# Optimization experiments

Hardware: AMD Instinct MI355X
Metric: run time of the kernel (lower is better)

The kernel has to match this reference:

```python
import jax, jax.numpy as jnp
import numpy as np

P_FACTOR = 3.0   # config['p_factor']
EPS = 1e-12      # torch F.normalize eps

def _l2_normalize(x):
    return x / jnp.maximum(jnp.linalg.norm(x, axis=-1, keepdims=True), EPS)

def _l1_normalize(x):
    return x / jnp.maximum(jnp.sum(jnp.abs(x), axis=-1, keepdims=True), EPS)

def setup_inputs() -> dict:
    key = jax.random.key(0)
    k = jax.random.split(key, 6)
    B, N_EX, D_IN, D_FEAT, N_LAB, D_CLS = 4096, 16384, 1024, 256, 28, 64
    features = jax.random.normal(k[0], (B, D_IN), jnp.float32)
    labels = jax.random.uniform(k[1], (B, N_LAB), jnp.float32)            # BCE targets in [0,1]
    ex_features = jax.random.normal(k[2], (N_EX, D_IN), jnp.float32)
    ex_classes = jax.random.uniform(k[3], (N_EX, N_LAB), jnp.float32)     # class memberships
    g_w = jax.random.normal(k[4], (D_FEAT, D_IN), jnp.float32) * 0.02     # Linear(in=1024,out=256,bias=False)
    class_reps = jax.random.uniform(k[5], (N_LAB, D_CLS), jnp.float32) * 2.0 - 1.0  # rand*2-1
    return {"features": features, "labels": labels, "ex_features": ex_features,
            "ex_classes": ex_classes, "g_w": g_w, "class_reps": class_reps}

def reference(features, labels, ex_features, ex_classes, g_w, class_reps):
    # g projection (use_g=True, no bias)
    f = features @ g_w.T          # [B, D_FEAT]
    ef = ex_features @ g_w.T      # [N_EX, D_FEAT]
    # exemplar class representations: L1-normalized memberships @ class_reps
    ex_class_reps = _l1_normalize(ex_classes) @ class_reps   # [N_EX, D_CLS]
    # cosine similarity between queries and exemplars
    s = _l2_normalize(f) @ _l2_normalize(ef).T               # [B, N_EX]
    # power-sign activation then L1 normalize over exemplars
    a = _l1_normalize(jnp.sign(s) * jnp.abs(s) ** P_FACTOR)  # [B, N_EX]
    # weighted exemplar aggregation
    echo = a @ ex_class_reps                                  # [B, D_CLS]
    # negative euclidean distances to class representations (cdist)
    diff = echo[:, None, :] - class_reps[None, :, :]          # [B, N_LAB, D_CLS]
    neg_dists = -jnp.sqrt(jnp.sum(diff * diff, axis=-1))      # [B, N_LAB]
    # BCEWithLogitsLoss (mean reduction)
    loss = jnp.mean(-(labels * jax.nn.log_sigmoid(neg_dists)
                      + (1.0 - labels) * jax.nn.log_sigmoid(-neg_dists)))
    return (loss, neg_dists)
```

## Files before the change

### kernel.cpp

```cpp
#include <hip/hip_runtime.h>


typedef __bf16 bf16x8 __attribute__((ext_vector_type(8)));
typedef __bf16 bf16x4 __attribute__((ext_vector_type(4)));
typedef float  f32x4  __attribute__((ext_vector_type(4)));

__device__ __forceinline__ f32x4 f4zero() { f32x4 z = {0.f, 0.f, 0.f, 0.f}; return z; }

__device__ __forceinline__ f32x4 mfma16(bf16x8 a, bf16x8 b, f32x4 c) {
  return __builtin_amdgcn_mfma_f32_16x16x32_bf16(a, b, c, 0, 0, 0);
}

__device__ __forceinline__ bf16x8 load8f(const float* p) {
  f32x4 a = *(const f32x4*)p;
  f32x4 b = *(const f32x4*)(p + 4);
  bf16x8 r;
  r[0] = (__bf16)a[0]; r[1] = (__bf16)a[1]; r[2] = (__bf16)a[2]; r[3] = (__bf16)a[3];
  r[4] = (__bf16)b[0]; r[5] = (__bf16)b[1]; r[6] = (__bf16)b[2]; r[7] = (__bf16)b[3];
  return r;
}

__device__ __forceinline__ void async16(const void* g, void* l) {
  __builtin_amdgcn_global_load_lds(
      (const __attribute__((address_space(1))) unsigned int*)g,
      (__attribute__((address_space(3))) unsigned int*)l, 16, 0, 0);
}

__device__ __forceinline__ void bar_lgkm() {
  asm volatile("s_waitcnt lgkmcnt(0)" ::: "memory");
  __builtin_amdgcn_s_barrier();
}
__device__ __forceinline__ void bar_all() {
  asm volatile("s_waitcnt vmcnt(0) lgkmcnt(0)" ::: "memory");
  __builtin_amdgcn_s_barrier();
}

__global__ void fill_sentinel(float* __restrict__ out, int n) {
  for (int i = blockIdx.x * 256 + threadIdx.x; i < n; i += gridDim.x * 256) out[i] = -1.0f;
}

__global__ void prep(const float* __restrict__ exc, __bf16* __restrict__ vT,
                     const float* __restrict__ W, __bf16* __restrict__ W2,
                     float* __restrict__ zp, int zn) {
  const int b = blockIdx.x, tid = threadIdx.x;
  if (b < 64) {
    int e = b * 256 + tid;
    float m[28];
    float s = 0.f;
#pragma unroll
    for (int j = 0; j < 28; j++) {
      m[j] = exc[(size_t)e * 28 + j];
      s += fabsf(m[j]);
    }
    float inv = 1.0f / fmaxf(s, 1e-12f);
#pragma unroll
    for (int j = 0; j < 28; j++) vT[(size_t)j * 16384 + e] = (__bf16)(m[j] * inv);
#pragma unroll
    for (int j = 28; j < 32; j++) vT[(size_t)j * 16384 + e] = (__bf16)0.0f;
  } else if (b < 192) {
    int i = (b - 64) * 256 + tid;
    int ks  = i >> 11;
    int idx = i & 2047;
    int row = idx >> 3;
    int c4  = (idx & 7) ^ (row & 7);
    *(bf16x8*)(W2 + (size_t)i * 8) = load8f(W + (size_t)row * 1024 + ks * 64 + c4 * 8);
  } else {
    for (int i = (b - 192) * 256 + tid; i < zn; i += (gridDim.x - 192) * 256) zp[i] = 0.f;
  }
}

__global__ __launch_bounds__(256, 2)
void proj_l2norm(const float* __restrict__ Xa, const float* __restrict__ Xb,
                 const __bf16* __restrict__ W2,
                 __bf16* __restrict__ Pa, __bf16* __restrict__ Pb) {
  __shared__ __align__(16) __bf16 Xs[2][32 * 72];
  __shared__ __align__(16) __bf16 Ws[2][256 * 64];
  __shared__ float nrmW[4 * 32];
  __shared__ float invn[32];

  const int tid = threadIdx.x;
  const int w = tid >> 6, lane = tid & 63;
  const int quad = lane >> 4, l15 = lane & 15;
  const int sw = l15 & 7;
  const int xrow = tid >> 3, xc8 = tid & 7;

  const float* X;
  __bf16* P;
  int row0;
  if (blockIdx.x < 512) { X = Xa; P = Pa; row0 = blockIdx.x * 32; }
  else                  { X = Xb; P = Pb; row0 = (blockIdx.x - 512) * 32; }

  const float* xsrc = X + (size_t)(row0 + xrow) * 1024 + xc8 * 8;

  *(bf16x8*)(&Xs[0][xrow * 72 + xc8 * 8]) = load8f(xsrc);
#pragma unroll
  for (int rep = 0; rep < 8; rep++) {
    int idx = rep * 256 + tid;
    async16(W2 + idx * 8, &Ws[0][idx * 8]);
  }

  f32x4 acc[2][4];
#pragma unroll
  for (int i = 0; i < 2; i++)
#pragma unroll
    for (int j = 0; j < 4; j++) acc[i][j] = f4zero();

  bar_all();

  int cur = 0;
  for (int ks = 0; ks < 16; ks++) {
    const int nxt = cur ^ 1;
    f32x4 xa, xb;
    if (ks < 15) {
      const float* xp = xsrc + (ks + 1) * 64;
      xa = *(const f32x4*)xp;
      xb = *(const f32x4*)(xp + 4);
      const __bf16* w2k = W2 + (size_t)(ks + 1) * 16384;
#pragma unroll
      for (int rep = 0; rep < 8; rep++) {
        int idx = rep * 256 + tid;
        async16(w2k + idx * 8, &Ws[nxt][idx * 8]);
      }
    }
#pragma unroll
    for (int ksub = 0; ksub < 2; ksub++) {
      bf16x8 af[2], bfr[4];
#pragma unroll
      for (int mb = 0; mb < 2; mb++)
        af[mb] = *(bf16x8*)(&Xs[cur][(mb * 16 + l15) * 72 + ksub * 32 + quad * 8]);
#pragma unroll
      for (int nb = 0; nb < 4; nb++) {
        int c4 = ksub * 4 + quad;
        bfr[nb] = *(bf16x8*)(&Ws[cur][(w * 64 + nb * 16 + l15) * 64 + (c4 ^ sw) * 8]);
      }
#pragma unroll
      for (int mb = 0; mb < 2; mb++)
#pragma unroll
        for (int nb = 0; nb < 4; nb++)
          acc[mb][nb] = mfma16(af[mb], bfr[nb], acc[mb][nb]);
    }
    if (ks < 15) {
      bf16x8 r;
      r[0] = (__bf16)xa[0]; r[1] = (__bf16)xa[1]; r[2] = (__bf16)xa[2]; r[3] = (__bf16)xa[3];
      r[4] = (__bf16)xb[0]; r[5] = (__bf16)xb[1]; r[6] = (__bf16)xb[2]; r[7] = (__bf16)xb[3];
      *(bf16x8*)(&Xs[nxt][xrow * 72 + xc8 * 8]) = r;
    }
    bar_all();
    cur = nxt;
  }

  float part[2][4];
#pragma unroll
  for (int mb = 0; mb < 2; mb++)
#pragma unroll
    for (int r = 0; r < 4; r++) {
      float s = 0.f;
#pragma unroll
      for (int nb = 0; nb < 4; nb++) { float v = acc[mb][nb][r]; s += v * v; }
      part[mb][r] = s;
    }
#pragma unroll
  for (int m = 1; m < 16; m <<= 1)
#pragma unroll
    for (int mb = 0; mb < 2; mb++)
#pragma unroll
      for (int r = 0; r < 4; r++) part[mb][r] += __shfl_xor(part[mb][r], m, 64);

  if (l15 == 0) {
#pragma unroll
    for (int mb = 0; mb < 2; mb++)
#pragma unroll
      for (int r = 0; r < 4; r++)
        nrmW[w * 32 + mb * 16 + quad * 4 + r] = part[mb][r];
  }
  __syncthreads();
  if (tid < 32) {
    float s = nrmW[tid] + nrmW[32 + tid] + nrmW[64 + tid] + nrmW[96 + tid];
    invn[tid] = 1.0f / fmaxf(sqrtf(s), 1e-12f);
  }
  __syncthreads();
#pragma unroll
  for (int mb = 0; mb < 2; mb++)
#pragma unroll
    for (int nb = 0; nb < 4; nb++)
#pragma unroll
      for (int r = 0; r < 4; r++) {
        int row = mb * 16 + quad * 4 + r;
        int col = w * 64 + nb * 16 + l15;
        P[(size_t)(row0 + row) * 256 + col] = (__bf16)(acc[mb][nb][r] * invn[row]);
      }
}

__global__ __launch_bounds__(256, 2)
void fused_sim(const __bf16* __restrict__ fn, const __bf16* __restrict__ efn,
               const __bf16* __restrict__ vTg,
               float* __restrict__ tT, float* __restrict__ r_acc) {
  __shared__ __align__(16) __bf16 Ks[64 * 256];
  __shared__ __align__(16) __bf16 Vs[2][32 * 64];
  __shared__ __align__(16) __bf16 Us[128 * 72];

  const int tid = threadIdx.x, w = tid >> 6, lane = tid & 63;
  const int quad = lane >> 4, l15 = lane & 15;
  const int wy = w >> 1, wx = w & 1;
  const int swk = l15 & 7;
  const int chunk = blockIdx.x & 15, mtile = blockIdx.x >> 4;
  const int q0 = mtile * 128;
  const int e_base = chunk * 1024;

  int koff[8];
#pragma unroll
  for (int rep = 0; rep < 8; rep++) {
    int idx = rep * 256 + tid;
    int row = idx >> 5;
    int c5  = (idx & 31) ^ (row & 7);
    koff[rep] = row * 256 + c5 * 8;
  }
  const int vrow = tid >> 3;
  const int vcs  = (tid & 7) ^ (vrow & 7);
  const size_t vsrc0 = (size_t)vrow * 16384 + e_base + vcs * 8;

  {
    const __bf16* src = efn + (size_t)e_base * 256;
#pragma unroll
    for (int rep = 0; rep < 8; rep++) async16(src + koff[rep], Ks + (rep * 256 + tid) * 8);
    async16(vTg + vsrc0, &Vs[0][tid * 8]);
  }

  bf16x8 qf[8][4];
#pragma unroll
  for (int ks = 0; ks < 8; ks++)
#pragma unroll
    for (int nb = 0; nb < 4; nb++)
      qf[ks][nb] = *(const bf16x8*)(fn + (size_t)(q0 + wx * 64 + nb * 16 + l15) * 256 +
                                    ks * 32 + quad * 8);

  float r_part[4] = {0.f, 0.f, 0.f, 0.f};
  f32x4 accp[2][2];
#pragma unroll
  for (int a = 0; a < 2; a++)
#pragma unroll
    for (int b = 0; b < 2; b++) accp[a][b] = f4zero();

  bar_all();

  int cur = 0;
  for (int t = 0; t < 16; t++) {
    f32x4 accs[2][4];
#pragma unroll
    for (int a = 0; a < 2; a++)
#pragma unroll
      for (int b = 0; b < 4; b++) accs[a][b] = f4zero();
#pragma unroll
    for (int ks = 0; ks < 8; ks++) {
      bf16x8 af[2];
#pragma unroll
      for (int mb = 0; mb < 2; mb++)
        af[mb] = *(bf16x8*)(Ks + (wy * 32 + mb * 16 + l15) * 256 +
                            ((ks * 4 + quad) ^ swk) * 8);
#pragma unroll
      for (int mb = 0; mb < 2; mb++)
#pragma unroll
        for (int nb = 0; nb < 4; nb++)
          accs[mb][nb] = mfma16(af[mb], qf[ks][nb], accs[mb][nb]);
    }

    bar_lgkm();

    if (t < 15) {
      const __bf16* src = efn + (size_t)(e_base + (t + 1) * 64) * 256;
#pragma unroll
      for (int rep = 0; rep < 8; rep++)
        async16(src + koff[rep], Ks + (rep * 256 + tid) * 8);
      async16(vTg + vsrc0 + (t + 1) * 64, &Vs[cur ^ 1][tid * 8]);
    }

#pragma unroll
    for (int mb = 0; mb < 2; mb++) {
      const int eo = wy * 32 + mb * 16 + quad * 4;
#pragma unroll
      for (int nb = 0; nb < 4; nb++) {
        const int q = wx * 64 + nb * 16 + l15;
        bf16x4 pk;
#pragma unroll
        for (int r = 0; r < 4; r++) {
          float s = accs[mb][nb][r];
          __bf16 ub = (__bf16)(s * s * s);
          pk[r] = ub;
          r_part[nb] += fabsf((float)ub);
        }
        *(bf16x4*)(Us + q * 72 + eo) = pk;
      }
    }

    bar_lgkm();

#pragma unroll
    for (int ks = 0; ks < 2; ks++) {
      bf16x8 vf[2], uf[2];
#pragma unroll
      for (int cb = 0; cb < 2; cb++)
        vf[cb] = *(bf16x8*)(&Vs[cur][(cb * 16 + l15) * 64 + ((ks * 4 + quad) ^ swk) * 8]);
#pragma unroll
      for (int qb = 0; qb < 2; qb++)
        uf[qb] = *(bf16x8*)(Us + (w * 32 + qb * 16 + l15) * 72 + ks * 32 + quad * 8);
#pragma unroll
      for (int cb = 0; cb < 2; cb++)
#pragma unroll
        for (int qb = 0; qb < 2; qb++)
          accp[cb][qb] = mfma16(vf[cb], uf[qb], accp[cb][qb]);
    }

    bar_all();
    cur ^= 1;
  }

#pragma unroll
  for (int nb = 0; nb < 4; nb++) {
    float v = r_part[nb];
    v += __shfl_xor(v, 16, 64);
    v += __shfl_xor(v, 32, 64);
    if (quad == 0) atomicAdd(&r_acc[q0 + wx * 64 + nb * 16 + l15], v);
  }
#pragma unroll
  for (int cb = 0; cb < 2; cb++)
#pragma unroll
    for (int qb = 0; qb < 2; qb++)
#pragma unroll
      for (int r = 0; r < 4; r++)
        atomicAdd(&tT[(size_t)(cb * 16 + quad * 4 + r) * 4096 + q0 + w * 32 + qb * 16 + l15],
                  accp[cb][qb][r]);
}

__global__ __launch_bounds__(256, 4)
void finalize(const float* __restrict__ tT, const float* __restrict__ r_acc,
              const float* __restrict__ creps, const float* __restrict__ labels,
              float* __restrict__ loss_acc, float* __restrict__ out) {
  __shared__ __align__(16) float cr[28 * 64];
  __shared__ float wsum[4];
  const int tid = threadIdx.x, w = tid >> 6, lane = tid & 63;
  for (int i = tid; i < 28 * 64; i += 256) cr[i] = creps[i];
  __syncthreads();

  const int q = blockIdx.x * 4 + w;
  float tval = 0.f;
  if (lane < 28) tval = tT[(size_t)lane * 4096 + q];
  tval *= 1.0f / fmaxf(r_acc[q], 1e-12f);

  float echo = 0.f;
#pragma unroll
  for (int j = 0; j < 28; j++)
    echo = fmaf(__shfl(tval, j, 64), cr[j * 64 + lane], echo);

  float dj = 0.f;
#pragma unroll
  for (int j = 0; j < 28; j++) {
    float df = echo - cr[j * 64 + lane];
    float d2 = df * df;
#pragma unroll
    for (int m = 1; m < 64; m <<= 1) d2 += __shfl_xor(d2, m, 64);
    if (lane == j) dj = sqrtf(d2);
  }

  float lsum = 0.f;
  if (lane < 28) {
    out[1 + (size_t)q * 28 + lane] = -dj;
    float y = labels[(size_t)q * 28 + lane];
    lsum = fmaf(y, dj, log1pf(expf(-dj)));
  }
#pragma unroll
  for (int m = 1; m < 64; m <<= 1) lsum += __shfl_xor(lsum, m, 64);
  if (lane == 0) wsum[w] = lsum;
  __syncthreads();
  if (tid == 0) atomicAdd(loss_acc, wsum[0] + wsum[1] + wsum[2] + wsum[3]);
}

__global__ void write_loss(const float* __restrict__ loss_acc, float* __restrict__ out) {
  out[0] = loss_acc[0] * (1.0f / 114688.0f);
}

extern "C" void kernel_launch(void* const* d_in, const int* in_sizes, int n_in,
                              void* d_out, int out_size, void* d_ws, size_t ws_size,
                              hipStream_t stream) {
  const float* features = nullptr;
  const float* labels   = nullptr;
  const float* ex_feat  = nullptr;
  const float* ex_cls   = nullptr;
  const float* g_w      = nullptr;
  const float* creps    = nullptr;
  for (int i = 0; i < n_in; i++) {
    switch (in_sizes[i]) {
      case 4194304:  features = (const float*)d_in[i]; break;
      case 114688:   labels   = (const float*)d_in[i]; break;
      case 16777216: ex_feat  = (const float*)d_in[i]; break;
      case 458752:   ex_cls   = (const float*)d_in[i]; break;
      case 262144:   g_w      = (const float*)d_in[i]; break;
      case 1792:     creps    = (const float*)d_in[i]; break;
      default: break;
    }
  }
  float* out = (float*)d_out;

  if (!features || !labels || !ex_feat || !ex_cls || !g_w || !creps ||
      ws_size < (16ull << 20)) {
    fill_sentinel<<<256, 256, 0, stream>>>(out, out_size);
    return;
  }

  char* ws = (char*)d_ws;
  __bf16* f_n   = (__bf16*)(ws);
  __bf16* ef_n  = (__bf16*)(ws + (2ull << 20));
  __bf16* vT    = (__bf16*)(ws + (10ull << 20));
  float*  tT    = (float*) (ws + (11ull << 20));
  float*  r_acc = tT + 32 * 4096;
  float*  lossp = r_acc + 4096;
  __bf16* W2    = (__bf16*)(ws + (12ull << 20));

  prep<<<720, 256, 0, stream>>>(ex_cls, vT, g_w, W2, tT, 32 * 4096 + 4096 + 1);

  proj_l2norm<<<640, 256, 0, stream>>>(ex_feat, features, W2, ef_n, f_n);
  fused_sim<<<512, 256, 0, stream>>>(f_n, ef_n, vT, tT, r_acc);
  finalize<<<1024, 256, 0, stream>>>(tT, r_acc, creps, labels, lossp, out);
  write_loss<<<1, 1, 0, stream>>>(lossp, out);
}
```

Baseline: 227.7 us.

## Read projection weights directly from global memory and fuse loss write into finalize

The projection kernel no longer stages the bf16 weight matrix through shared memory with async copies. Each wave now reads its 64-row weight strip straight from global memory (L2-resident), and the K loop uses 128-wide steps with a smaller X tile. The smaller shared footprint lets the launch bounds ask for 3 blocks per CU. The swizzled W2 layout is dropped for a plain row-major bf16 copy. The separate write_loss launch is replaced by a last-block atomic counter inside finalize. This trades LDS reuse of the weights for more global/L2 traffic per wave in exchange for higher occupancy and one fewer launch.

```diff
diff --git a/kernel.cpp b/kernel.cpp
--- a/kernel.cpp
+++ b/kernel.cpp
@@ -14,6 +14,13 @@
 __device__ __forceinline__ bf16x8 load8f(const float* p) {
   f32x4 a = *(const f32x4*)p;
   f32x4 b = *(const f32x4*)(p + 4);
+  bf16x8 r;
+  r[0] = (__bf16)a[0]; r[1] = (__bf16)a[1]; r[2] = (__bf16)a[2]; r[3] = (__bf16)a[3];
+  r[4] = (__bf16)b[0]; r[5] = (__bf16)b[1]; r[6] = (__bf16)b[2]; r[7] = (__bf16)b[3];
+  return r;
+}
+
+__device__ __forceinline__ bf16x8 cvt2(f32x4 a, f32x4 b) {
   bf16x8 r;
   r[0] = (__bf16)a[0]; r[1] = (__bf16)a[1]; r[2] = (__bf16)a[2]; r[3] = (__bf16)a[3];
   r[4] = (__bf16)b[0]; r[5] = (__bf16)b[1]; r[6] = (__bf16)b[2]; r[7] = (__bf16)b[3];
@@ -59,30 +66,24 @@
     for (int j = 28; j < 32; j++) vT[(size_t)j * 16384 + e] = (__bf16)0.0f;
   } else if (b < 192) {
     int i = (b - 64) * 256 + tid;
-    int ks  = i >> 11;
-    int idx = i & 2047;
-    int row = idx >> 3;
-    int c4  = (idx & 7) ^ (row & 7);
-    *(bf16x8*)(W2 + (size_t)i * 8) = load8f(W + (size_t)row * 1024 + ks * 64 + c4 * 8);
+    *(bf16x8*)(W2 + (size_t)i * 8) = load8f(W + (size_t)i * 8);
   } else {
     for (int i = (b - 192) * 256 + tid; i < zn; i += (gridDim.x - 192) * 256) zp[i] = 0.f;
   }
 }
 
-__global__ __launch_bounds__(256, 2)
+__global__ __launch_bounds__(256, 3)
 void proj_l2norm(const float* __restrict__ Xa, const float* __restrict__ Xb,
                  const __bf16* __restrict__ W2,
                  __bf16* __restrict__ Pa, __bf16* __restrict__ Pb) {
-  __shared__ __align__(16) __bf16 Xs[2][32 * 72];
-  __shared__ __align__(16) __bf16 Ws[2][256 * 64];
+  __shared__ __align__(16) __bf16 Xs[2][32 * 136];
   __shared__ float nrmW[4 * 32];
   __shared__ float invn[32];
 
   const int tid = threadIdx.x;
   const int w = tid >> 6, lane = tid & 63;
   const int quad = lane >> 4, l15 = lane & 15;
-  const int sw = l15 & 7;
-  const int xrow = tid >> 3, xc8 = tid & 7;
+  const int srow = tid >> 4, sc = tid & 15;
 
   const float* X;
   __bf16* P;
@@ -90,14 +91,11 @@
   if (blockIdx.x < 512) { X = Xa; P = Pa; row0 = blockIdx.x * 32; }
   else                  { X = Xb; P = Pb; row0 = (blockIdx.x - 512) * 32; }
 
-  const float* xsrc = X + (size_t)(row0 + xrow) * 1024 + xc8 * 8;
-
-  *(bf16x8*)(&Xs[0][xrow * 72 + xc8 * 8]) = load8f(xsrc);
-#pragma unroll
-  for (int rep = 0; rep < 8; rep++) {
-    int idx = rep * 256 + tid;
-    async16(W2 + idx * 8, &Ws[0][idx * 8]);
-  }
+  const float* xp0 = X + (size_t)(row0 + srow) * 1024 + sc * 8;
+  const float* xp1 = xp0 + (size_t)16 * 1024;
+
+  *(bf16x8*)(&Xs[0][srow * 136 + sc * 8])        = load8f(xp0);
+  *(bf16x8*)(&Xs[0][(srow + 16) * 136 + sc * 8]) = load8f(xp1);
 
   f32x4 acc[2][4];
 #pragma unroll
@@ -105,47 +103,41 @@
 #pragma unroll
     for (int j = 0; j < 4; j++) acc[i][j] = f4zero();
 
-  bar_all();
+  const __bf16* wstrip = W2 + (size_t)(w * 64) * 1024;
+
+  __syncthreads();
 
   int cur = 0;
-  for (int ks = 0; ks < 16; ks++) {
+  for (int kb = 0; kb < 8; kb++) {
     const int nxt = cur ^ 1;
-    f32x4 xa, xb;
-    if (ks < 15) {
-      const float* xp = xsrc + (ks + 1) * 64;
-      xa = *(const f32x4*)xp;
-      xb = *(const f32x4*)(xp + 4);
-      const __bf16* w2k = W2 + (size_t)(ks + 1) * 16384;
-#pragma unroll
-      for (int rep = 0; rep < 8; rep++) {
-        int idx = rep * 256 + tid;
-        async16(w2k + idx * 8, &Ws[nxt][idx * 8]);
-      }
-    }
-#pragma unroll
-    for (int ksub = 0; ksub < 2; ksub++) {
+    f32x4 p00, p01, p10, p11;
+    if (kb < 7) {
+      const float* q0 = xp0 + (kb + 1) * 128;
+      const float* q1 = xp1 + (kb + 1) * 128;
+      p00 = *(const f32x4*)q0; p01 = *(const f32x4*)(q0 + 4);
+      p10 = *(const f32x4*)q1; p11 = *(const f32x4*)(q1 + 4);
+    }
+    const __bf16* wk = wstrip + kb * 128;
+#pragma unroll
+    for (int ksub = 0; ksub < 4; ksub++) {
       bf16x8 af[2], bfr[4];
 #pragma unroll
       for (int mb = 0; mb < 2; mb++)
-        af[mb] = *(bf16x8*)(&Xs[cur][(mb * 16 + l15) * 72 + ksub * 32 + quad * 8]);
-#pragma unroll
-      for (int nb = 0; nb < 4; nb++) {
-        int c4 = ksub * 4 + quad;
-        bfr[nb] = *(bf16x8*)(&Ws[cur][(w * 64 + nb * 16 + l15) * 64 + (c4 ^ sw) * 8]);
-      }
+        af[mb] = *(bf16x8*)(&Xs[cur][(mb * 16 + l15) * 136 + ksub * 32 + quad * 8]);
+#pragma unroll
+      for (int nb = 0; nb < 4; nb++)
+        bfr[nb] = *(const bf16x8*)(wk + (size_t)(nb * 16 + l15) * 1024 + ksub * 32 + quad * 8);
 #pragma unroll
       for (int mb = 0; mb < 2; mb++)
 #pragma unroll
         for (int nb = 0; nb < 4; nb++)
           acc[mb][nb] = mfma16(af[mb], bfr[nb], acc[mb][nb]);
     }
-    if (ks < 15) {
-      bf16x8 r;
-      r[0] = (__bf16)xa[0]; r[1] = (__bf16)xa[1]; r[2] = (__bf16)xa[2]; r[3] = (__bf16)xa[3];
-      r[4] = (__bf16)xb[0]; r[5] = (__bf16)xb[1]; r[6] = (__bf16)xb[2]; r[7] = (__bf16)xb[3];
-      *(bf16x8*)(&Xs[nxt][xrow * 72 + xc8 * 8]) = r;
-    }
-    bar_all();
+    if (kb < 7) {
+      *(bf16x8*)(&Xs[nxt][srow * 136 + sc * 8])        = cvt2(p00, p01);
+      *(bf16x8*)(&Xs[nxt][(srow + 16) * 136 + sc * 8]) = cvt2(p10, p11);
+    }
+    __syncthreads();
     cur = nxt;
   }
 
@@ -371,11 +363,16 @@
   for (int m = 1; m < 64; m <<= 1) lsum += __shfl_xor(lsum, m, 64);
   if (lane == 0) wsum[w] = lsum;
   __syncthreads();
-  if (tid == 0) atomicAdd(loss_acc, wsum[0] + wsum[1] + wsum[2] + wsum[3]);
-}
-
-__global__ void write_loss(const float* __restrict__ loss_acc, float* __restrict__ out) {
-  out[0] = loss_acc[0] * (1.0f / 114688.0f);
+  if (tid == 0) {
+    atomicAdd(loss_acc, wsum[0] + wsum[1] + wsum[2] + wsum[3]);
+    __threadfence();
+    unsigned* cnt = (unsigned*)(loss_acc + 1);
+    unsigned old = atomicAdd(cnt, 1u);
+    if (old == gridDim.x - 1) {
+      float total = atomicAdd(loss_acc, 0.0f);
+      out[0] = total * (1.0f / 114688.0f);
+    }
+  }
 }
 
 extern "C" void kernel_launch(void* const* d_in, const int* in_sizes, int n_in,
@@ -415,10 +412,9 @@
   float*  lossp = r_acc + 4096;
   __bf16* W2    = (__bf16*)(ws + (12ull << 20));
 
-  prep<<<720, 256, 0, stream>>>(ex_cls, vT, g_w, W2, tT, 32 * 4096 + 4096 + 1);
+  prep<<<720, 256, 0, stream>>>(ex_cls, vT, g_w, W2, tT, 32 * 4096 + 4096 + 2);
 
   proj_l2norm<<<640, 256, 0, stream>>>(ex_feat, features, W2, ef_n, f_n);
   fused_sim<<<512, 256, 0, stream>>>(f_n, ef_n, vT, tT, r_acc);
   finalize<<<1024, 256, 0, stream>>>(tT, r_acc, creps, labels, lossp, out);
-  write_loss<<<1, 1, 0, stream>>>(lossp, out);
-}
+}
```

Measured after the change: 240.3 us. 1.06x slower.
